# Kernel tuning notes

Measured on AMD Instinct MI355X. Metric: run time of the kernel, lower is better.

## Reference

```python
import jax, jax.numpy as jnp
import numpy as np

B, N, FN, FE = 8, 256, 64, 64  # batch, nodes, node feat, edge feat


def gnn_layer(A, x, e, We, be, Wn, bn):
    # A: [B,N,N] float mask, x: [B,N,Fn], e: [B,N,N,Fe_in]
    b, n, fn = x.shape
    xi = jnp.broadcast_to(x[:, :, None, :], (b, n, n, fn))  # sender feats
    xj = jnp.broadcast_to(x[:, None, :, :], (b, n, n, fn))  # receiver feats
    h = jnp.concatenate([xi, xj, e], axis=-1)               # [B,N,N,2Fn+Fe]
    e_new = jax.nn.relu(jnp.einsum('bijk,kf->bijf', h, We) + be) * A[..., None]
    deg = jnp.clip(jnp.sum(A, axis=2), 1.0, None)           # [B,N]
    agg = jnp.sum(e_new, axis=2) / deg[..., None]           # mean over neighbors
    x_new = jax.nn.relu(jnp.concatenate([x, agg], axis=-1) @ Wn + bn)
    return x_new, e_new


def setup_inputs() -> dict:
    key = jax.random.key(0)
    ks = jax.random.split(key, 20)
    s = 0.05
    inp = {
        'edge_index': jax.random.randint(ks[0], (B, N, N), 0, 2, dtype=jnp.int32),
        'x': jax.random.normal(ks[1], (B, N, FN), dtype=jnp.float32),
        'edge_attr': jax.random.normal(ks[2], (B, N, N, FE), dtype=jnp.float32),
    }
    # 3 GNN layers: edge-update MLP (2Fn+Fe -> Fe) and node-update (Fn+Fe -> Fn)
    for l in range(3):
        inp[f'We{l}'] = jax.random.normal(ks[3 + 4 * l], (2 * FN + FE, FE), jnp.float32) * s
        inp[f'be{l}'] = jnp.zeros((FE,), jnp.float32)
        inp[f'Wn{l}'] = jax.random.normal(ks[4 + 4 * l], (FN + FE, FN), jnp.float32) * s
        inp[f'bn{l}'] = jnp.zeros((FN,), jnp.float32)
    # spectral-norm MLP head: Fe -> Fe -> Fe -> 1
    inp['W1'] = jax.random.normal(ks[15], (FE, FE), jnp.float32) * s
    inp['b1'] = jnp.zeros((FE,), jnp.float32)
    inp['W2'] = jax.random.normal(ks[16], (FE, FE), jnp.float32) * s
    inp['b2'] = jnp.zeros((FE,), jnp.float32)
    inp['W3'] = jax.random.normal(ks[17], (FE, 1), jnp.float32) * s
    inp['b3'] = jnp.zeros((1,), jnp.float32)
    return inp


def reference(edge_index, x, edge_attr,
              We0, be0, Wn0, bn0,
              We1, be1, Wn1, bn1,
              We2, be2, Wn2, bn2,
              W1, b1, W2, b2, W3, b3):
    A = edge_index.astype(jnp.float32)
    x = x.astype(jnp.float32)
    # layer 0 updates both nodes and edges
    x1, e = gnn_layer(A, x, edge_attr, We0, be0, Wn0, bn0)
    # middle layer(s): node output discarded (as in original forward)
    _, e = gnn_layer(A, x1, e, We1, be1, Wn1, bn1)
    # last layer
    _, edges = gnn_layer(A, x1, e, We2, be2, Wn2, bn2)
    # end == 'edge_mean'
    v = jnp.mean(edges, axis=(1, 2))  # [B, FE]
    h = jax.nn.relu(v @ W1 + b1)
    h = jax.nn.relu(h @ W2 + b2)
    out = h @ W3 + b3                  # [B, 1]
    return jnp.squeeze(out, axis=-1)   # [B]
```

## Files before the change

### kernel.cpp

```cpp
#include <hip/hip_runtime.h>

#define BB 8
#define NN 256
#define FF 64
#define ET 128

__global__ __launch_bounds__(256) void pq_kernel(
    const float* __restrict__ x, const float* __restrict__ We,
    const float* __restrict__ be, float* __restrict__ P, float* __restrict__ Q,
    float* __restrict__ agg)
{
    const int rl = threadIdx.x >> 6, f = threadIdx.x & 63;
    const int r = blockIdx.x * 4 + rl;
    __shared__ float xs[4][FF];
    xs[rl][f] = x[r * FF + f];
    agg[r * FF + f] = 0.f;
    __syncthreads();
    float p = be[f], q = 0.f;
#pragma unroll
    for (int k = 0; k < FF; ++k) {
        const float xv = xs[rl][k];
        p = fmaf(xv, We[k * FF + f], p);
        q = fmaf(xv, We[(FF + k) * FF + f], q);
    }
    P[r * FF + f] = p;
    Q[r * FF + f] = q;
}

__global__ __launch_bounds__(256) void edge0_kernel(
    const float* __restrict__ e_in, const float* __restrict__ Wc,
    const float* __restrict__ P, const float* __restrict__ Q,
    const int* __restrict__ A, float* __restrict__ e_out,
    float* __restrict__ agg)
{
    __shared__ float Wl[FF * FF];
    __shared__ float el[FF * ET];
    __shared__ float Al[ET];
    __shared__ float Pl[FF];
    __shared__ float red[FF];

    const int tid = threadIdx.x;
    const int bt  = blockIdx.x;
    const int bi  = bt >> 1;
    const int b   = bi >> 8;
    const int j0  = (bt & 1) << 7;

    {
        const float4* Ws = (const float4*)Wc;
        float4*       Wd = (float4*)Wl;
#pragma unroll
        for (int m = 0; m < 4; ++m) Wd[tid + m * 256] = Ws[tid + m * 256];
    }
    if (tid < ET) Al[tid] = (float)A[bi * NN + j0 + tid];
    if (tid < FF) Pl[tid] = P[bi * FF + tid];

    {
        const int et = tid >> 1, kh = (tid & 1) * 32;
        const float4* src = (const float4*)(e_in + ((size_t)bi * NN + j0 + et) * FF + kh);
        float4 v[8];
#pragma unroll
        for (int i = 0; i < 8; ++i) v[i] = src[i];
#pragma unroll
        for (int i = 0; i < 8; ++i) {
            el[(kh + 4 * i + 0) * ET + et] = v[i].x;
            el[(kh + 4 * i + 1) * ET + et] = v[i].y;
            el[(kh + 4 * i + 2) * ET + et] = v[i].z;
            el[(kh + 4 * i + 3) * ET + et] = v[i].w;
        }
    }
    __syncthreads();

    const int tj = tid & 31, tf = tid >> 5;
    const int f0 = tf * 8;

    float acc[4][8];
#pragma unroll
    for (int a = 0; a < 4; ++a)
#pragma unroll
        for (int c = 0; c < 8; ++c) acc[a][c] = 0.f;

#pragma unroll 8
    for (int k = 0; k < FF; ++k) {
        const float4 w0 = *(const float4*)&Wl[k * FF + f0];
        const float4 w1 = *(const float4*)&Wl[k * FF + f0 + 4];
        const float wv[8] = {w0.x, w0.y, w0.z, w0.w, w1.x, w1.y, w1.z, w1.w};
#pragma unroll
        for (int m = 0; m < 2; ++m) {
            const float2 ev = *(const float2*)&el[k * ET + 2 * tj + 64 * m];
#pragma unroll
            for (int ff = 0; ff < 8; ++ff) {
                acc[2 * m][ff]     = fmaf(ev.x, wv[ff], acc[2 * m][ff]);
                acc[2 * m + 1][ff] = fmaf(ev.y, wv[ff], acc[2 * m + 1][ff]);
            }
        }
    }

    float psum[8];
#pragma unroll
    for (int ff = 0; ff < 8; ++ff) psum[ff] = 0.f;
    const float* Qb = Q + (size_t)b * NN * FF;
#pragma unroll
    for (int m = 0; m < 2; ++m)
#pragma unroll
        for (int p = 0; p < 2; ++p) {
            const int ee = 2 * tj + 64 * m + p;
            const int jj = 2 * m + p;
            const int j  = j0 + ee;
            const float a = Al[ee];
            const float4 q0 = *(const float4*)(Qb + j * FF + f0);
            const float4 q1 = *(const float4*)(Qb + j * FF + f0 + 4);
            const float qv[8] = {q0.x, q0.y, q0.z, q0.w, q1.x, q1.y, q1.z, q1.w};
            float r[8];
#pragma unroll
            for (int ff = 0; ff < 8; ++ff) {
                r[ff] = fmaxf(acc[jj][ff] + Pl[f0 + ff] + qv[ff], 0.f) * a;
                psum[ff] += r[ff];
            }
            float* orow = e_out + ((size_t)bi * NN + j) * FF;
            *(float4*)(orow + f0)     = make_float4(r[0], r[1], r[2], r[3]);
            *(float4*)(orow + f0 + 4) = make_float4(r[4], r[5], r[6], r[7]);
        }
#pragma unroll
    for (int ff = 0; ff < 8; ++ff) {
#pragma unroll
        for (int off = 16; off > 0; off >>= 1)
            psum[ff] += __shfl_down(psum[ff], off, 32);
    }
    if (tj == 0) {
#pragma unroll
        for (int ff = 0; ff < 8; ++ff) red[f0 + ff] = psum[ff];
    }
    __syncthreads();
    if (tid < FF) atomicAdd(&agg[bi * FF + tid], red[tid]);
}

__global__ __launch_bounds__(256) void nodepq_kernel(
    const float* __restrict__ x, const float* __restrict__ agg,
    const int* __restrict__ A,
    const float* __restrict__ Wn, const float* __restrict__ bn,
    const float* __restrict__ We1, const float* __restrict__ be1,
    const float* __restrict__ We2, const float* __restrict__ be2,
    float* __restrict__ P1, float* __restrict__ Q1,
    float* __restrict__ P2, float* __restrict__ Q2, float* __restrict__ v)
{
    const int rl = threadIdx.x >> 6, f = threadIdx.x & 63;
    const int r = blockIdx.x * 4 + rl;
    __shared__ float s[4][2 * FF];
    __shared__ float x1s[4][FF];

    float da = (float)A[r * NN + f] + (float)A[r * NN + f + 64] +
               (float)A[r * NN + f + 128] + (float)A[r * NN + f + 192];
#pragma unroll
    for (int off = 32; off > 0; off >>= 1) da += __shfl_down(da, off, 64);
    const float deg = fmaxf(__shfl(da, 0, 64), 1.0f);

    s[rl][f]      = x[r * FF + f];
    s[rl][FF + f] = agg[r * FF + f] / deg;
    if (blockIdx.x == 0) {
        v[threadIdx.x] = 0.f;
        v[256 + threadIdx.x] = 0.f;
    }
    __syncthreads();
    float a = bn[f];
#pragma unroll
    for (int k = 0; k < 2 * FF; ++k) a = fmaf(s[rl][k], Wn[k * FF + f], a);
    x1s[rl][f] = fmaxf(a, 0.f);
    __syncthreads();
    float p1 = be1[f], q1 = 0.f, p2 = be2[f], q2 = 0.f;
#pragma unroll
    for (int k = 0; k < FF; ++k) {
        const float xv = x1s[rl][k];
        p1 = fmaf(xv, We1[k * FF + f], p1);
        q1 = fmaf(xv, We1[(FF + k) * FF + f], q1);
        p2 = fmaf(xv, We2[k * FF + f], p2);
        q2 = fmaf(xv, We2[(FF + k) * FF + f], q2);
    }
    P1[r * FF + f] = p1;  Q1[r * FF + f] = q1;
    P2[r * FF + f] = p2;  Q2[r * FF + f] = q2;
}

__global__ __launch_bounds__(256) void edge12_kernel(
    const float* __restrict__ e_in,
    const float* __restrict__ Wc1, const float* __restrict__ Wc2,
    const float* __restrict__ P1, const float* __restrict__ Q1,
    const float* __restrict__ P2, const float* __restrict__ Q2,
    const int* __restrict__ A, float* __restrict__ v)
{
    __shared__ float Wl[FF * FF];
    __shared__ float el[FF * ET];
    __shared__ float Al[ET];
    __shared__ float Pl1[FF], Pl2[FF];
    __shared__ float red[FF];

    const int tid = threadIdx.x;
    const int bt  = blockIdx.x;
    const int bi  = bt >> 1;
    const int b   = bi >> 8;
    const int j0  = (bt & 1) << 7;

    {
        const float4* Ws = (const float4*)Wc1;
        float4*       Wd = (float4*)Wl;
#pragma unroll
        for (int m = 0; m < 4; ++m) Wd[tid + m * 256] = Ws[tid + m * 256];
    }
    if (tid < ET) Al[tid] = (float)A[bi * NN + j0 + tid];
    if (tid < FF) { Pl1[tid] = P1[bi * FF + tid]; Pl2[tid] = P2[bi * FF + tid]; }

    {
        const int et = tid >> 1, kh = (tid & 1) * 32;
        const float4* src = (const float4*)(e_in + ((size_t)bi * NN + j0 + et) * FF + kh);
        float4 vv[8];
#pragma unroll
        for (int i = 0; i < 8; ++i) vv[i] = src[i];
#pragma unroll
        for (int i = 0; i < 8; ++i) {
            el[(kh + 4 * i + 0) * ET + et] = vv[i].x;
            el[(kh + 4 * i + 1) * ET + et] = vv[i].y;
            el[(kh + 4 * i + 2) * ET + et] = vv[i].z;
            el[(kh + 4 * i + 3) * ET + et] = vv[i].w;
        }
    }
    __syncthreads();

    const int tj = tid & 31, tf = tid >> 5;
    const int f0 = tf * 8;

    float acc[4][8];
#pragma unroll
    for (int a = 0; a < 4; ++a)
#pragma unroll
        for (int c = 0; c < 8; ++c) acc[a][c] = 0.f;

#pragma unroll 8
    for (int k = 0; k < FF; ++k) {
        const float4 w0 = *(const float4*)&Wl[k * FF + f0];
        const float4 w1 = *(const float4*)&Wl[k * FF + f0 + 4];
        const float wv[8] = {w0.x, w0.y, w0.z, w0.w, w1.x, w1.y, w1.z, w1.w};
#pragma unroll
        for (int m = 0; m < 2; ++m) {
            const float2 ev = *(const float2*)&el[k * ET + 2 * tj + 64 * m];
#pragma unroll
            for (int ff = 0; ff < 8; ++ff) {
                acc[2 * m][ff]     = fmaf(ev.x, wv[ff], acc[2 * m][ff]);
                acc[2 * m + 1][ff] = fmaf(ev.y, wv[ff], acc[2 * m + 1][ff]);
            }
        }
    }

    {
        const float* Q1b = Q1 + (size_t)b * NN * FF;
#pragma unroll
        for (int m = 0; m < 2; ++m)
#pragma unroll
            for (int p = 0; p < 2; ++p) {
                const int ee = 2 * tj + 64 * m + p;
                const int jj = 2 * m + p;
                const int j  = j0 + ee;
                const float a = Al[ee];
                const float4 q0 = *(const float4*)(Q1b + j * FF + f0);
                const float4 q1 = *(const float4*)(Q1b + j * FF + f0 + 4);
                const float qv[8] = {q0.x, q0.y, q0.z, q0.w, q1.x, q1.y, q1.z, q1.w};
#pragma unroll
                for (int ff = 0; ff < 8; ++ff)
                    acc[jj][ff] = fmaxf(acc[jj][ff] + Pl1[f0 + ff] + qv[ff], 0.f) * a;
            }
    }
    __syncthreads();

    {
        const float4* Ws = (const float4*)Wc2;
        float4*       Wd = (float4*)Wl;
#pragma unroll
        for (int m = 0; m < 4; ++m) Wd[tid + m * 256] = Ws[tid + m * 256];
    }
#pragma unroll
    for (int ff = 0; ff < 8; ++ff)
#pragma unroll
        for (int m = 0; m < 2; ++m)
            *(float2*)&el[(f0 + ff) * ET + 2 * tj + 64 * m] =
                make_float2(acc[2 * m][ff], acc[2 * m + 1][ff]);
    __syncthreads();

    float acc2[4][8];
#pragma unroll
    for (int a = 0; a < 4; ++a)
#pragma unroll
        for (int c = 0; c < 8; ++c) acc2[a][c] = 0.f;

#pragma unroll 8
    for (int k = 0; k < FF; ++k) {
        const float4 w0 = *(const float4*)&Wl[k * FF + f0];
        const float4 w1 = *(const float4*)&Wl[k * FF + f0 + 4];
        const float wv[8] = {w0.x, w0.y, w0.z, w0.w, w1.x, w1.y, w1.z, w1.w};
#pragma unroll
        for (int m = 0; m < 2; ++m) {
            const float2 ev = *(const float2*)&el[k * ET + 2 * tj + 64 * m];
#pragma unroll
            for (int ff = 0; ff < 8; ++ff) {
                acc2[2 * m][ff]     = fmaf(ev.x, wv[ff], acc2[2 * m][ff]);
                acc2[2 * m + 1][ff] = fmaf(ev.y, wv[ff], acc2[2 * m + 1][ff]);
            }
        }
    }

    float psum[8];
#pragma unroll
    for (int ff = 0; ff < 8; ++ff) psum[ff] = 0.f;
    const float* Q2b = Q2 + (size_t)b * NN * FF;
#pragma unroll
    for (int m = 0; m < 2; ++m)
#pragma unroll
        for (int p = 0; p < 2; ++p) {
            const int ee = 2 * tj + 64 * m + p;
            const int jj = 2 * m + p;
            const int j  = j0 + ee;
            const float a = Al[ee];
            const float4 q0 = *(const float4*)(Q2b + j * FF + f0);
            const float4 q1 = *(const float4*)(Q2b + j * FF + f0 + 4);
            const float qv[8] = {q0.x, q0.y, q0.z, q0.w, q1.x, q1.y, q1.z, q1.w};
#pragma unroll
            for (int ff = 0; ff < 8; ++ff)
                psum[ff] += fmaxf(acc2[jj][ff] + Pl2[f0 + ff] + qv[ff], 0.f) * a;
        }
#pragma unroll
    for (int ff = 0; ff < 8; ++ff) {
#pragma unroll
        for (int off = 16; off > 0; off >>= 1)
            psum[ff] += __shfl_down(psum[ff], off, 32);
    }
    if (tj == 0) {
#pragma unroll
        for (int ff = 0; ff < 8; ++ff) red[f0 + ff] = psum[ff];
    }
    __syncthreads();
    if (tid < FF) atomicAdd(&v[b * FF + tid], red[tid]);
}

__global__ __launch_bounds__(64) void head_kernel(
    const float* __restrict__ vsum, const float* __restrict__ W1,
    const float* __restrict__ b1, const float* __restrict__ W2,
    const float* __restrict__ b2, const float* __restrict__ W3,
    const float* __restrict__ b3, float* __restrict__ out)
{
    const int f = threadIdx.x;
    __shared__ float hv[BB][FF];
    __shared__ float h1[BB][FF];
#pragma unroll
    for (int b = 0; b < BB; ++b) hv[b][f] = vsum[b * FF + f] * (1.0f / 65536.0f);
    __syncthreads();
#pragma unroll
    for (int b = 0; b < BB; ++b) {
        float acc = b1[f];
#pragma unroll
        for (int k = 0; k < FF; ++k) acc = fmaf(hv[b][k], W1[k * FF + f], acc);
        h1[b][f] = fmaxf(acc, 0.f);
    }
    __syncthreads();
#pragma unroll
    for (int b = 0; b < BB; ++b) {
        float acc = b2[f];
#pragma unroll
        for (int k = 0; k < FF; ++k) acc = fmaf(h1[b][k], W2[k * FF + f], acc);
        hv[b][f] = fmaxf(acc, 0.f);
    }
    __syncthreads();
#pragma unroll
    for (int b = 0; b < BB; ++b) {
        float p = hv[b][f] * W3[f];
#pragma unroll
        for (int off = 32; off > 0; off >>= 1) p += __shfl_down(p, off);
        if (f == 0) out[b] = p + b3[0];
    }
}

extern "C" void kernel_launch(void* const* d_in, const int* in_sizes, int n_in,
                              void* d_out, int out_size, void* d_ws, size_t ws_size,
                              hipStream_t stream)
{
    const int*   A      = (const int*)d_in[0];
    const float* x      = (const float*)d_in[1];
    float*       e_attr = (float*)d_in[2];

    const float* We0 = (const float*)d_in[3];
    const float* be0 = (const float*)d_in[4];
    const float* Wn0 = (const float*)d_in[5];
    const float* bn0 = (const float*)d_in[6];
    const float* We1 = (const float*)d_in[7];
    const float* be1 = (const float*)d_in[8];
    const float* We2 = (const float*)d_in[11];
    const float* be2 = (const float*)d_in[12];
    const float* W1 = (const float*)d_in[15];
    const float* b1 = (const float*)d_in[16];
    const float* W2 = (const float*)d_in[17];
    const float* b2 = (const float*)d_in[18];
    const float* W3 = (const float*)d_in[19];
    const float* b3 = (const float*)d_in[20];
    float* out = (float*)d_out;
    (void)in_sizes; (void)n_in; (void)out_size; (void)ws_size;

    const int R = BB * NN;
    float* P1  = (float*)d_ws;
    float* Q1  = P1 + R * FF;
    float* P2  = Q1 + R * FF;
    float* Q2  = P2 + R * FF;
    float* agg = Q2 + R * FF;
    float* v   = agg + R * FF;

    const int EB = 2 * R;

    pq_kernel<<<R / 4, 256, 0, stream>>>(x, We0, be0, P1, Q1, agg);
    edge0_kernel<<<EB, 256, 0, stream>>>(e_attr, We0 + 2 * FF * FF, P1, Q1, A,
                                         e_attr, agg);
    nodepq_kernel<<<R / 4, 256, 0, stream>>>(x, agg, A, Wn0, bn0, We1, be1,
                                             We2, be2, P1, Q1, P2, Q2, v);
    edge12_kernel<<<EB, 256, 0, stream>>>(e_attr, We1 + 2 * FF * FF,
                                          We2 + 2 * FF * FF, P1, Q1, P2, Q2, A, v);
    head_kernel<<<1, 64, 0, stream>>>(v, W1, b1, W2, b2, W3, b3, out);
}
```

Baseline: 414.2 us.

## Use bf16 MFMA with hi/lo split weights for edge MLP matmuls

Replaces the scalar FP32 FMA inner products in edge0 and edge12 with 16x16x32 bf16 MFMA instructions. Activations are rounded to bf16, and the weights are split into bf16 high and low parts by a new prep kernel that writes a swizzled layout to limit LDS bank conflicts. The intermediate edge tensor in edge12 is kept in LDS as bf16. This targets the FP32 ALU cost and the large shared-memory transpose staging of edge features. In exchange it loses accuracy, because the edge activations are truncated to bf16.

```diff
diff --git a/kernel.cpp b/kernel.cpp
--- a/kernel.cpp
+++ b/kernel.cpp
@@ -3,7 +3,46 @@
 #define BB 8
 #define NN 256
 #define FF 64
-#define ET 128
+
+typedef float f32x4 __attribute__((ext_vector_type(4)));
+typedef short s16x8 __attribute__((ext_vector_type(8)));
+typedef unsigned short u16;
+
+#define MFMA_BF16(a, b, c) __builtin_amdgcn_mfma_f32_16x16x32_bf16(a, b, c, 0, 0, 0)
+
+__device__ inline u16 f2bf(float x) {
+    unsigned u = __float_as_uint(x);
+    u += 0x7FFFu + ((u >> 16) & 1u);
+    return (u16)(u >> 16);
+}
+__device__ inline float bf2f(u16 h) { return __uint_as_float(((unsigned)h) << 16); }
+
+__device__ inline s16x8 cvt_a(float4 v0, float4 v1) {
+    s16x8 a;
+    a[0] = (short)f2bf(v0.x); a[1] = (short)f2bf(v0.y);
+    a[2] = (short)f2bf(v0.z); a[3] = (short)f2bf(v0.w);
+    a[4] = (short)f2bf(v1.x); a[5] = (short)f2bf(v1.y);
+    a[6] = (short)f2bf(v1.z); a[7] = (short)f2bf(v1.w);
+    return a;
+}
+
+__global__ __launch_bounds__(256) void wprep_kernel(
+    const float* __restrict__ We0, const float* __restrict__ We1,
+    const float* __restrict__ We2, u16* __restrict__ wimg)
+{
+    const float* src =
+        (blockIdx.x == 0 ? We0 : (blockIdx.x == 1 ? We1 : We2)) + 2 * FF * FF;
+    u16* hi = wimg + blockIdx.x * 8192;
+    u16* lo = hi + 4096;
+    for (int idx = threadIdx.x; idx < 4096; idx += 256) {
+        const int f = idx >> 6, rem = idx & 63, cs = rem >> 3, j = rem & 7;
+        const int k = ((cs ^ (f & 7)) << 3) | j;
+        const float wv = src[k * FF + f];
+        const u16 h = f2bf(wv);
+        hi[idx] = h;
+        lo[idx] = f2bf(wv - bf2f(h));
+    }
+}
 
 __global__ __launch_bounds__(256) void pq_kernel(
     const float* __restrict__ x, const float* __restrict__ We,
@@ -28,16 +67,13 @@
 }
 
 __global__ __launch_bounds__(256) void edge0_kernel(
-    const float* __restrict__ e_in, const float* __restrict__ Wc,
-    const float* __restrict__ P, const float* __restrict__ Q,
-    const int* __restrict__ A, float* __restrict__ e_out,
-    float* __restrict__ agg)
-{
-    __shared__ float Wl[FF * FF];
-    __shared__ float el[FF * ET];
-    __shared__ float Al[ET];
-    __shared__ float Pl[FF];
-    __shared__ float red[FF];
+    const float* __restrict__ e_in, const u16* __restrict__ whi,
+    const u16* __restrict__ wlo, const float* __restrict__ P,
+    const float* __restrict__ Q, const int* __restrict__ A,
+    float* __restrict__ e_out, float* __restrict__ agg)
+{
+    __shared__ u16 Whl[4096], Wll[4096];
+    __shared__ float Al[128], Pl[64];
 
     const int tid = threadIdx.x;
     const int bt  = blockIdx.x;
@@ -45,93 +81,87 @@
     const int b   = bi >> 8;
     const int j0  = (bt & 1) << 7;
 
-    {
-        const float4* Ws = (const float4*)Wc;
-        float4*       Wd = (float4*)Wl;
-#pragma unroll
-        for (int m = 0; m < 4; ++m) Wd[tid + m * 256] = Ws[tid + m * 256];
-    }
-    if (tid < ET) Al[tid] = (float)A[bi * NN + j0 + tid];
-    if (tid < FF) Pl[tid] = P[bi * FF + tid];
-
-    {
-        const int et = tid >> 1, kh = (tid & 1) * 32;
-        const float4* src = (const float4*)(e_in + ((size_t)bi * NN + j0 + et) * FF + kh);
-        float4 v[8];
-#pragma unroll
-        for (int i = 0; i < 8; ++i) v[i] = src[i];
-#pragma unroll
-        for (int i = 0; i < 8; ++i) {
-            el[(kh + 4 * i + 0) * ET + et] = v[i].x;
-            el[(kh + 4 * i + 1) * ET + et] = v[i].y;
-            el[(kh + 4 * i + 2) * ET + et] = v[i].z;
-            el[(kh + 4 * i + 3) * ET + et] = v[i].w;
-        }
-    }
-    __syncthreads();
-
-    const int tj = tid & 31, tf = tid >> 5;
-    const int f0 = tf * 8;
-
-    float acc[4][8];
-#pragma unroll
-    for (int a = 0; a < 4; ++a)
-#pragma unroll
-        for (int c = 0; c < 8; ++c) acc[a][c] = 0.f;
-
-#pragma unroll 8
-    for (int k = 0; k < FF; ++k) {
-        const float4 w0 = *(const float4*)&Wl[k * FF + f0];
-        const float4 w1 = *(const float4*)&Wl[k * FF + f0 + 4];
-        const float wv[8] = {w0.x, w0.y, w0.z, w0.w, w1.x, w1.y, w1.z, w1.w};
-#pragma unroll
-        for (int m = 0; m < 2; ++m) {
-            const float2 ev = *(const float2*)&el[k * ET + 2 * tj + 64 * m];
-#pragma unroll
-            for (int ff = 0; ff < 8; ++ff) {
-                acc[2 * m][ff]     = fmaf(ev.x, wv[ff], acc[2 * m][ff]);
-                acc[2 * m + 1][ff] = fmaf(ev.y, wv[ff], acc[2 * m + 1][ff]);
-            }
-        }
-    }
-
-    float psum[8];
-#pragma unroll
-    for (int ff = 0; ff < 8; ++ff) psum[ff] = 0.f;
+#pragma unroll
+    for (int m = 0; m < 2; ++m) {
+        ((uint4*)Whl)[tid + 256 * m] = ((const uint4*)whi)[tid + 256 * m];
+        ((uint4*)Wll)[tid + 256 * m] = ((const uint4*)wlo)[tid + 256 * m];
+    }
+    if (tid < 128) Al[tid] = (float)A[bi * NN + j0 + tid];
+    if (tid < 64)  Pl[tid] = P[bi * FF + tid];
+
+    const int w = tid >> 6, lane = tid & 63;
+    const int quad = lane >> 4, l15 = lane & 15, l7 = lane & 7;
+    const int e_base = 32 * w;
+
+    const float* erow = e_in + ((size_t)bi * NN + j0) * FF;
+
+    s16x8 afr[2][2];
+#pragma unroll
+    for (int ks = 0; ks < 2; ++ks)
+#pragma unroll
+        for (int et = 0; et < 2; ++et) {
+            const float* p = erow + (e_base + et * 16 + l15) * FF + ks * 32 + quad * 8;
+            afr[ks][et] = cvt_a(*(const float4*)p, *(const float4*)(p + 4));
+        }
+
+    float qv[2][4][4];
     const float* Qb = Q + (size_t)b * NN * FF;
 #pragma unroll
-    for (int m = 0; m < 2; ++m)
-#pragma unroll
-        for (int p = 0; p < 2; ++p) {
-            const int ee = 2 * tj + 64 * m + p;
-            const int jj = 2 * m + p;
-            const int j  = j0 + ee;
-            const float a = Al[ee];
-            const float4 q0 = *(const float4*)(Qb + j * FF + f0);
-            const float4 q1 = *(const float4*)(Qb + j * FF + f0 + 4);
-            const float qv[8] = {q0.x, q0.y, q0.z, q0.w, q1.x, q1.y, q1.z, q1.w};
-            float r[8];
-#pragma unroll
-            for (int ff = 0; ff < 8; ++ff) {
-                r[ff] = fmaxf(acc[jj][ff] + Pl[f0 + ff] + qv[ff], 0.f) * a;
-                psum[ff] += r[ff];
-            }
-            float* orow = e_out + ((size_t)bi * NN + j) * FF;
-            *(float4*)(orow + f0)     = make_float4(r[0], r[1], r[2], r[3]);
-            *(float4*)(orow + f0 + 4) = make_float4(r[4], r[5], r[6], r[7]);
-        }
-#pragma unroll
-    for (int ff = 0; ff < 8; ++ff) {
-#pragma unroll
-        for (int off = 16; off > 0; off >>= 1)
-            psum[ff] += __shfl_down(psum[ff], off, 32);
-    }
-    if (tj == 0) {
-#pragma unroll
-        for (int ff = 0; ff < 8; ++ff) red[f0 + ff] = psum[ff];
-    }
-    __syncthreads();
-    if (tid < FF) atomicAdd(&agg[bi * FF + tid], red[tid]);
+    for (int et = 0; et < 2; ++et)
+#pragma unroll
+        for (int ft = 0; ft < 4; ++ft)
+#pragma unroll
+            for (int r = 0; r < 4; ++r)
+                qv[et][ft][r] =
+                    Qb[(j0 + e_base + et * 16 + quad * 4 + r) * FF + ft * 16 + l15];
+
+    __syncthreads();
+
+    f32x4 acc[2][4];
+#pragma unroll
+    for (int et = 0; et < 2; ++et)
+#pragma unroll
+        for (int ft = 0; ft < 4; ++ft) acc[et][ft] = (f32x4){0.f, 0.f, 0.f, 0.f};
+
+#pragma unroll
+    for (int ks = 0; ks < 2; ++ks)
+#pragma unroll
+        for (int ft = 0; ft < 4; ++ft) {
+            const int f  = ft * 16 + l15;
+            const int ca = (ks * 4 + quad) ^ l7;
+            const s16x8 bh = *(const s16x8*)&Whl[f * 64 + ca * 8];
+            const s16x8 bl = *(const s16x8*)&Wll[f * 64 + ca * 8];
+#pragma unroll
+            for (int et = 0; et < 2; ++et) {
+                acc[et][ft] = MFMA_BF16(afr[ks][et], bh, acc[et][ft]);
+                acc[et][ft] = MFMA_BF16(afr[ks][et], bl, acc[et][ft]);
+            }
+        }
+
+    float psum[4] = {0.f, 0.f, 0.f, 0.f};
+#pragma unroll
+    for (int et = 0; et < 2; ++et)
+#pragma unroll
+        for (int ft = 0; ft < 4; ++ft)
+#pragma unroll
+            for (int r = 0; r < 4; ++r) {
+                const int el = e_base + et * 16 + quad * 4 + r;
+                const int f  = ft * 16 + l15;
+                const float val = acc[et][ft][r] + Pl[f] + qv[et][ft][r];
+                const float rv  = fmaxf(val, 0.f) * Al[el];
+                e_out[((size_t)bi * NN + j0 + el) * FF + f] = rv;
+                psum[ft] += rv;
+            }
+#pragma unroll
+    for (int ft = 0; ft < 4; ++ft) {
+        psum[ft] += __shfl_down(psum[ft], 32);
+        psum[ft] += __shfl_down(psum[ft], 16);
+    }
+    if (lane < 16) {
+#pragma unroll
+        for (int ft = 0; ft < 4; ++ft)
+            atomicAdd(&agg[bi * FF + ft * 16 + l15], psum[ft]);
+    }
 }
 
 __global__ __launch_bounds__(256) void nodepq_kernel(
@@ -181,16 +211,15 @@
 
 __global__ __launch_bounds__(256) void edge12_kernel(
     const float* __restrict__ e_in,
-    const float* __restrict__ Wc1, const float* __restrict__ Wc2,
+    const u16* __restrict__ w1hi, const u16* __restrict__ w1lo,
+    const u16* __restrict__ w2hi, const u16* __restrict__ w2lo,
     const float* __restrict__ P1, const float* __restrict__ Q1,
     const float* __restrict__ P2, const float* __restrict__ Q2,
     const int* __restrict__ A, float* __restrict__ v)
 {
-    __shared__ float Wl[FF * FF];
-    __shared__ float el[FF * ET];
-    __shared__ float Al[ET];
-    __shared__ float Pl1[FF], Pl2[FF];
-    __shared__ float red[FF];
+    __shared__ u16 W1h[4096], W1l[4096], W2h[4096], W2l[4096];
+    __shared__ u16 E2[128 * 64];
+    __shared__ float Al[128], Pl1[64], Pl2[64], red[64];
 
     const int tid = threadIdx.x;
     const int bt  = blockIdx.x;
@@ -198,143 +227,152 @@
     const int b   = bi >> 8;
     const int j0  = (bt & 1) << 7;
 
-    {
-        const float4* Ws = (const float4*)Wc1;
-        float4*       Wd = (float4*)Wl;
-#pragma unroll
-        for (int m = 0; m < 4; ++m) Wd[tid + m * 256] = Ws[tid + m * 256];
-    }
-    if (tid < ET) Al[tid] = (float)A[bi * NN + j0 + tid];
-    if (tid < FF) { Pl1[tid] = P1[bi * FF + tid]; Pl2[tid] = P2[bi * FF + tid]; }
-
-    {
-        const int et = tid >> 1, kh = (tid & 1) * 32;
-        const float4* src = (const float4*)(e_in + ((size_t)bi * NN + j0 + et) * FF + kh);
-        float4 vv[8];
-#pragma unroll
-        for (int i = 0; i < 8; ++i) vv[i] = src[i];
-#pragma unroll
-        for (int i = 0; i < 8; ++i) {
-            el[(kh + 4 * i + 0) * ET + et] = vv[i].x;
-            el[(kh + 4 * i + 1) * ET + et] = vv[i].y;
-            el[(kh + 4 * i + 2) * ET + et] = vv[i].z;
-            el[(kh + 4 * i + 3) * ET + et] = vv[i].w;
-        }
-    }
-    __syncthreads();
-
-    const int tj = tid & 31, tf = tid >> 5;
-    const int f0 = tf * 8;
-
-    float acc[4][8];
-#pragma unroll
-    for (int a = 0; a < 4; ++a)
-#pragma unroll
-        for (int c = 0; c < 8; ++c) acc[a][c] = 0.f;
-
-#pragma unroll 8
-    for (int k = 0; k < FF; ++k) {
-        const float4 w0 = *(const float4*)&Wl[k * FF + f0];
-        const float4 w1 = *(const float4*)&Wl[k * FF + f0 + 4];
-        const float wv[8] = {w0.x, w0.y, w0.z, w0.w, w1.x, w1.y, w1.z, w1.w};
-#pragma unroll
-        for (int m = 0; m < 2; ++m) {
-            const float2 ev = *(const float2*)&el[k * ET + 2 * tj + 64 * m];
-#pragma unroll
-            for (int ff = 0; ff < 8; ++ff) {
-                acc[2 * m][ff]     = fmaf(ev.x, wv[ff], acc[2 * m][ff]);
-                acc[2 * m + 1][ff] = fmaf(ev.y, wv[ff], acc[2 * m + 1][ff]);
-            }
-        }
-    }
-
+#pragma unroll
+    for (int m = 0; m < 2; ++m) {
+        ((uint4*)W1h)[tid + 256 * m] = ((const uint4*)w1hi)[tid + 256 * m];
+        ((uint4*)W1l)[tid + 256 * m] = ((const uint4*)w1lo)[tid + 256 * m];
+        ((uint4*)W2h)[tid + 256 * m] = ((const uint4*)w2hi)[tid + 256 * m];
+        ((uint4*)W2l)[tid + 256 * m] = ((const uint4*)w2lo)[tid + 256 * m];
+    }
+    if (tid < 128) Al[tid] = (float)A[bi * NN + j0 + tid];
+    if (tid < 64) {
+        Pl1[tid] = P1[bi * FF + tid];
+        Pl2[tid] = P2[bi * FF + tid];
+        red[tid] = 0.f;
+    }
+
+    const int w = tid >> 6, lane = tid & 63;
+    const int quad = lane >> 4, l15 = lane & 15, l7 = lane & 7;
+    const int e_base = 32 * w;
+
+    const float* erow = e_in + ((size_t)bi * NN + j0) * FF;
+
+    s16x8 afr[2][2];
+#pragma unroll
+    for (int ks = 0; ks < 2; ++ks)
+#pragma unroll
+        for (int et = 0; et < 2; ++et) {
+            const float* p = erow + (e_base + et * 16 + l15) * FF + ks * 32 + quad * 8;
+            afr[ks][et] = cvt_a(*(const float4*)p, *(const float4*)(p + 4));
+        }
+
+    float qv[2][4][4];
     {
         const float* Q1b = Q1 + (size_t)b * NN * FF;
 #pragma unroll
-        for (int m = 0; m < 2; ++m)
-#pragma unroll
-            for (int p = 0; p < 2; ++p) {
-                const int ee = 2 * tj + 64 * m + p;
-                const int jj = 2 * m + p;
-                const int j  = j0 + ee;
-                const float a = Al[ee];
-                const float4 q0 = *(const float4*)(Q1b + j * FF + f0);
-                const float4 q1 = *(const float4*)(Q1b + j * FF + f0 + 4);
-                const float qv[8] = {q0.x, q0.y, q0.z, q0.w, q1.x, q1.y, q1.z, q1.w};
-#pragma unroll
-                for (int ff = 0; ff < 8; ++ff)
-                    acc[jj][ff] = fmaxf(acc[jj][ff] + Pl1[f0 + ff] + qv[ff], 0.f) * a;
-            }
-    }
-    __syncthreads();
+        for (int et = 0; et < 2; ++et)
+#pragma unroll
+            for (int ft = 0; ft < 4; ++ft)
+#pragma unroll
+                for (int r = 0; r < 4; ++r)
+                    qv[et][ft][r] =
+                        Q1b[(j0 + e_base + et * 16 + quad * 4 + r) * FF + ft * 16 + l15];
+    }
+
+    __syncthreads();
+
+    f32x4 acc[2][4];
+#pragma unroll
+    for (int et = 0; et < 2; ++et)
+#pragma unroll
+        for (int ft = 0; ft < 4; ++ft) acc[et][ft] = (f32x4){0.f, 0.f, 0.f, 0.f};
+
+#pragma unroll
+    for (int ks = 0; ks < 2; ++ks)
+#pragma unroll
+        for (int ft = 0; ft < 4; ++ft) {
+            const int f  = ft * 16 + l15;
+            const int ca = (ks * 4 + quad) ^ l7;
+            const s16x8 bh = *(const s16x8*)&W1h[f * 64 + ca * 8];
+            const s16x8 bl = *(const s16x8*)&W1l[f * 64 + ca * 8];
+#pragma unroll
+            for (int et = 0; et < 2; ++et) {
+                acc[et][ft] = MFMA_BF16(afr[ks][et], bh, acc[et][ft]);
+                acc[et][ft] = MFMA_BF16(afr[ks][et], bl, acc[et][ft]);
+            }
+        }
+
+#pragma unroll
+    for (int et = 0; et < 2; ++et)
+#pragma unroll
+        for (int ft = 0; ft < 4; ++ft)
+#pragma unroll
+            for (int r = 0; r < 4; ++r) {
+                const int el = e_base + et * 16 + quad * 4 + r;
+                const int f  = ft * 16 + l15;
+                const float val = acc[et][ft][r] + Pl1[f] + qv[et][ft][r];
+                const float rv  = fmaxf(val, 0.f) * Al[el];
+                const int c  = f >> 3;
+                const int cs = c ^ (el & 7);
+                E2[el * 64 + cs * 8 + l7] = f2bf(rv);
+            }
 
     {
-        const float4* Ws = (const float4*)Wc2;
-        float4*       Wd = (float4*)Wl;
-#pragma unroll
-        for (int m = 0; m < 4; ++m) Wd[tid + m * 256] = Ws[tid + m * 256];
-    }
-#pragma unroll
-    for (int ff = 0; ff < 8; ++ff)
-#pragma unroll
-        for (int m = 0; m < 2; ++m)
-            *(float2*)&el[(f0 + ff) * ET + 2 * tj + 64 * m] =
-                make_float2(acc[2 * m][ff], acc[2 * m + 1][ff]);
-    __syncthreads();
-
-    float acc2[4][8];
-#pragma unroll
-    for (int a = 0; a < 4; ++a)
-#pragma unroll
-        for (int c = 0; c < 8; ++c) acc2[a][c] = 0.f;
-
-#pragma unroll 8
-    for (int k = 0; k < FF; ++k) {
-        const float4 w0 = *(const float4*)&Wl[k * FF + f0];
-        const float4 w1 = *(const float4*)&Wl[k * FF + f0 + 4];
-        const float wv[8] = {w0.x, w0.y, w0.z, w0.w, w1.x, w1.y, w1.z, w1.w};
-#pragma unroll
-        for (int m = 0; m < 2; ++m) {
-            const float2 ev = *(const float2*)&el[k * ET + 2 * tj + 64 * m];
-#pragma unroll
-            for (int ff = 0; ff < 8; ++ff) {
-                acc2[2 * m][ff]     = fmaf(ev.x, wv[ff], acc2[2 * m][ff]);
-                acc2[2 * m + 1][ff] = fmaf(ev.y, wv[ff], acc2[2 * m + 1][ff]);
-            }
-        }
-    }
-
-    float psum[8];
-#pragma unroll
-    for (int ff = 0; ff < 8; ++ff) psum[ff] = 0.f;
-    const float* Q2b = Q2 + (size_t)b * NN * FF;
-#pragma unroll
-    for (int m = 0; m < 2; ++m)
-#pragma unroll
-        for (int p = 0; p < 2; ++p) {
-            const int ee = 2 * tj + 64 * m + p;
-            const int jj = 2 * m + p;
-            const int j  = j0 + ee;
-            const float a = Al[ee];
-            const float4 q0 = *(const float4*)(Q2b + j * FF + f0);
-            const float4 q1 = *(const float4*)(Q2b + j * FF + f0 + 4);
-            const float qv[8] = {q0.x, q0.y, q0.z, q0.w, q1.x, q1.y, q1.z, q1.w};
-#pragma unroll
-            for (int ff = 0; ff < 8; ++ff)
-                psum[ff] += fmaxf(acc2[jj][ff] + Pl2[f0 + ff] + qv[ff], 0.f) * a;
-        }
-#pragma unroll
-    for (int ff = 0; ff < 8; ++ff) {
-#pragma unroll
-        for (int off = 16; off > 0; off >>= 1)
-            psum[ff] += __shfl_down(psum[ff], off, 32);
-    }
-    if (tj == 0) {
-#pragma unroll
-        for (int ff = 0; ff < 8; ++ff) red[f0 + ff] = psum[ff];
-    }
-    __syncthreads();
-    if (tid < FF) atomicAdd(&v[b * FF + tid], red[tid]);
+        const float* Q2b = Q2 + (size_t)b * NN * FF;
+#pragma unroll
+        for (int et = 0; et < 2; ++et)
+#pragma unroll
+            for (int ft = 0; ft < 4; ++ft)
+#pragma unroll
+                for (int r = 0; r < 4; ++r)
+                    qv[et][ft][r] =
+                        Q2b[(j0 + e_base + et * 16 + quad * 4 + r) * FF + ft * 16 + l15];
+    }
+
+    __syncthreads();
+
+#pragma unroll
+    for (int et = 0; et < 2; ++et)
+#pragma unroll
+        for (int ft = 0; ft < 4; ++ft) acc[et][ft] = (f32x4){0.f, 0.f, 0.f, 0.f};
+
+#pragma unroll
+    for (int ks = 0; ks < 2; ++ks) {
+        s16x8 a2[2];
+#pragma unroll
+        for (int et = 0; et < 2; ++et) {
+            const int e  = e_base + et * 16 + l15;
+            const int ca = (ks * 4 + quad) ^ l7;
+            a2[et] = *(const s16x8*)&E2[e * 64 + ca * 8];
+        }
+#pragma unroll
+        for (int ft = 0; ft < 4; ++ft) {
+            const int f  = ft * 16 + l15;
+            const int ca = (ks * 4 + quad) ^ l7;
+            const s16x8 bh = *(const s16x8*)&W2h[f * 64 + ca * 8];
+            const s16x8 bl = *(const s16x8*)&W2l[f * 64 + ca * 8];
+#pragma unroll
+            for (int et = 0; et < 2; ++et) {
+                acc[et][ft] = MFMA_BF16(a2[et], bh, acc[et][ft]);
+                acc[et][ft] = MFMA_BF16(a2[et], bl, acc[et][ft]);
+            }
+        }
+    }
+
+    float psum[4] = {0.f, 0.f, 0.f, 0.f};
+#pragma unroll
+    for (int et = 0; et < 2; ++et)
+#pragma unroll
+        for (int ft = 0; ft < 4; ++ft)
+#pragma unroll
+            for (int r = 0; r < 4; ++r) {
+                const int el = e_base + et * 16 + quad * 4 + r;
+                const int f  = ft * 16 + l15;
+                const float val = acc[et][ft][r] + Pl2[f] + qv[et][ft][r];
+                psum[ft] += fmaxf(val, 0.f) * Al[el];
+            }
+#pragma unroll
+    for (int ft = 0; ft < 4; ++ft) {
+        psum[ft] += __shfl_down(psum[ft], 32);
+        psum[ft] += __shfl_down(psum[ft], 16);
+    }
+    if (lane < 16) {
+#pragma unroll
+        for (int ft = 0; ft < 4; ++ft)
+            atomicAdd(&red[ft * 16 + l15], psum[ft]);
+    }
+    __syncthreads();
+    if (tid < 64) atomicAdd(&v[b * FF + tid], red[tid]);
 }
 
 __global__ __launch_bounds__(64) void head_kernel(
@@ -406,15 +444,19 @@
     float* Q2  = P2 + R * FF;
     float* agg = Q2 + R * FF;
     float* v   = agg + R * FF;
+    u16*  wimg = (u16*)(v + 512);
 
     const int EB = 2 * R;
 
+    wprep_kernel<<<3, 256, 0, stream>>>(We0, We1, We2, wimg);
     pq_kernel<<<R / 4, 256, 0, stream>>>(x, We0, be0, P1, Q1, agg);
-    edge0_kernel<<<EB, 256, 0, stream>>>(e_attr, We0 + 2 * FF * FF, P1, Q1, A,
+    edge0_kernel<<<EB, 256, 0, stream>>>(e_attr, wimg, wimg + 4096, P1, Q1, A,
                                          e_attr, agg);
     nodepq_kernel<<<R / 4, 256, 0, stream>>>(x, agg, A, Wn0, bn0, We1, be1,
                                              We2, be2, P1, Q1, P2, Q2, v);
-    edge12_kernel<<<EB, 256, 0, stream>>>(e_attr, We1 + 2 * FF * FF,
-                                          We2 + 2 * FF * FF, P1, Q1, P2, Q2, A, v);
+    edge12_kernel<<<EB, 256, 0, stream>>>(e_attr,
+                                          wimg + 8192, wimg + 12288,
+                                          wimg + 16384, wimg + 20480,
+                                          P1, Q1, P2, Q2, A, v);
     head_kernel<<<1, 64, 0, stream>>>(v, W1, b1, W2, b2, W3, b3, out);
 }
```

After: 361.7 us. -12.7%, faster.
